# Optimization experiments

Measured on AMD Instinct MI355X. Metric: run time of the kernel, lower is better.

Reference implementation:

```python
import jax, jax.numpy as jnp
import numpy as np

N = 100000   # nodes
E = 1600000  # edges (avg degree 16)
D_IN = 128
H = 256
D_OUT = 128


def setup_inputs() -> dict:
    key = jax.random.key(0)
    ks = jax.random.split(key, 12)

    def lin_w(k, fan_in, fan_out):
        # torch nn.Linear-style uniform init
        bound = 1.0 / np.sqrt(fan_in)
        return jax.random.uniform(k, (fan_in, fan_out), jnp.float32, -bound, bound)

    return {
        "in_feat": jax.random.normal(ks[0], (N, D_IN), jnp.float32),
        "src": jax.random.randint(ks[1], (E,), 0, N, jnp.int32),
        "dst": jax.random.randint(ks[2], (E,), 0, N, jnp.int32),
        "Wc0": lin_w(ks[3], D_IN, H), "bc0": jnp.zeros((H,), jnp.float32),
        "Wc1": lin_w(ks[4], H, H),    "bc1": jnp.zeros((H,), jnp.float32),
        "Wc2": lin_w(ks[5], H, D_OUT),"bc2": jnp.zeros((D_OUT,), jnp.float32),
        "Wr0": lin_w(ks[6], D_OUT, H),"br0": jnp.zeros((H,), jnp.float32),
        "Wr1": lin_w(ks[7], H, H),    "br1": jnp.zeros((H,), jnp.float32),
        "Wr2": lin_w(ks[8], H, D_IN), "br2": jnp.zeros((D_IN,), jnp.float32),
    }


def _graph_conv(h, src, dst, W, b):
    """DGL GraphConv, norm='both': D_out^{-1/2} A D_in^{-1/2} h W + b."""
    ones = jnp.ones(src.shape[0], h.dtype)
    out_deg = jnp.clip(jax.ops.segment_sum(ones, src, num_segments=N), 1.0)
    in_deg = jnp.clip(jax.ops.segment_sum(ones, dst, num_segments=N), 1.0)
    h = h * (out_deg ** -0.5)[:, None]
    h = h @ W                                    # transform before aggregate
    h = jax.ops.segment_sum(h[src], dst, num_segments=N)  # SpMM aggregation
    return h * (in_deg ** -0.5)[:, None] + b


def reference(in_feat, src, dst, Wc0, bc0, Wc1, bc1, Wc2, bc2,
              Wr0, br0, Wr1, br1, Wr2, br2):
    h = jnp.tanh(_graph_conv(in_feat, src, dst, Wc0, bc0))
    h = jnp.tanh(_graph_conv(h, src, dst, Wc1, bc1))
    h = jax.nn.softmax(_graph_conv(h, src, dst, Wc2, bc2), axis=1)
    r = jnp.tanh(h @ Wr0 + br0)
    r = jnp.tanh(r @ Wr1 + br1)
    r = jax.nn.softmax(r @ Wr2 + br2, axis=1)
    return (h, r)
```

## Files before the change

### kernel.cpp

```cpp
#include <hip/hip_runtime.h>

typedef __attribute__((ext_vector_type(8))) short short8;
typedef __attribute__((ext_vector_type(4))) float f32x4;

__device__ __forceinline__ ushort f2bf(float v) {
    unsigned u = __builtin_bit_cast(unsigned, v);
    unsigned r = (u + 0x7FFFu + ((u >> 16) & 1u)) >> 16;
    return (ushort)r;
}
__device__ __forceinline__ float lo16(unsigned p) { return __builtin_bit_cast(float, p << 16); }
__device__ __forceinline__ float hi16(unsigned p) { return __builtin_bit_cast(float, p & 0xFFFF0000u); }

__device__ __forceinline__ float fast_tanh(float x) {
    float cx = fminf(fmaxf(x, -9.f), 9.f);
    float e = __expf(2.f * cx);
    return (e - 1.f) / (e + 1.f);
}

__device__ __forceinline__ void async16(const void* g, void* l) {
    __builtin_amdgcn_global_load_lds(
        (const __attribute__((address_space(1))) unsigned*)g,
        (__attribute__((address_space(3))) unsigned*)l, 16, 0, 0);
}

#define BSHIFT 9
#define CHUNK 4096

__global__ __launch_bounds__(256) void bucket_count(const int* __restrict__ src,
        const int* __restrict__ dst, int* __restrict__ gbc,
        int* __restrict__ outc, int E) {
    __shared__ int cnt[256];
    int t = threadIdx.x;
    cnt[t] = 0;
    __syncthreads();
    int start = blockIdx.x * CHUNK;
    int n = E - start; if (n > CHUNK) n = CHUNK;
#pragma unroll
    for (int k = 0; k < CHUNK / 256; ++k) {
        int i = t + k * 256;
        if (i < n) {
            atomicAdd(&cnt[dst[start + i] >> BSHIFT], 1);
            atomicAdd(&outc[src[start + i]], 1);
        }
    }
    __syncthreads();
    if (cnt[t]) atomicAdd(&gbc[t], cnt[t]);
}

__global__ void scan_buckets(const int* __restrict__ gbc, int* __restrict__ bucketBase,
                             int* __restrict__ pairCursor, int* __restrict__ roff,
                             int N, int E) {
    __shared__ int s[256];
    int t = threadIdx.x;
    int v = gbc[t];
    s[t] = v; __syncthreads();
    for (int o = 1; o < 256; o <<= 1) {
        int y = (t >= o) ? s[t - o] : 0;
        __syncthreads();
        s[t] += y;
        __syncthreads();
    }
    int excl = s[t] - v;
    bucketBase[t] = excl;
    pairCursor[t] = excl;
    if (t == 255) bucketBase[256] = s[255];
    if (t == 0) roff[N] = E;
}

__global__ __launch_bounds__(256) void part_scatter(const int* __restrict__ src,
        const int* __restrict__ dst, int* __restrict__ pairCursor,
        uint2* __restrict__ pairs, int E) {
    __shared__ int cnt[256];
    __shared__ int base[256];
    int t = threadIdx.x;
    cnt[t] = 0;
    __syncthreads();
    int start = blockIdx.x * CHUNK;
    int n = E - start; if (n > CHUNK) n = CHUNK;
    int sv[CHUNK / 256], dv[CHUNK / 256], rk[CHUNK / 256], bk[CHUNK / 256];
#pragma unroll
    for (int k = 0; k < CHUNK / 256; ++k) {
        int i = t + k * 256;
        if (i < n) {
            sv[k] = src[start + i];
            dv[k] = dst[start + i];
            bk[k] = dv[k] >> BSHIFT;
            rk[k] = atomicAdd(&cnt[bk[k]], 1);
        } else bk[k] = -1;
    }
    __syncthreads();
    base[t] = cnt[t] ? atomicAdd(&pairCursor[t], cnt[t]) : 0;
    __syncthreads();
#pragma unroll
    for (int k = 0; k < CHUNK / 256; ++k)
        if (bk[k] >= 0) pairs[base[bk[k]] + rk[k]] = make_uint2((unsigned)sv[k], (unsigned)dv[k]);
}

__global__ __launch_bounds__(256) void build_bucket(const uint2* __restrict__ pairs,
        const int* __restrict__ bucketBase, int* __restrict__ roff,
        float* __restrict__ sIn, int* __restrict__ csr, int N) {
    __shared__ int cnt[512];
    __shared__ int cur[512];
    __shared__ int ss[256];
    int b = blockIdx.x;
    int t = threadIdx.x;
    int lo = b << BSHIFT;
    int s0 = bucketBase[b], s1 = bucketBase[b + 1];
    cnt[t] = 0; cnt[t + 256] = 0;
    __syncthreads();
    for (int j = s0 + t; j < s1; j += 256)
        atomicAdd(&cnt[pairs[j].y - lo], 1);
    __syncthreads();
    int c0 = cnt[2 * t], c1 = cnt[2 * t + 1];
    ss[t] = c0 + c1; __syncthreads();
    for (int o = 1; o < 256; o <<= 1) {
        int y = (t >= o) ? ss[t - o] : 0;
        __syncthreads();
        ss[t] += y;
        __syncthreads();
    }
    int eb = ss[t] - (c0 + c1);
    int p0 = s0 + eb, p1 = s0 + eb + c0;
    cur[2 * t] = p0; cur[2 * t + 1] = p1;
    int n0 = lo + 2 * t, n1 = n0 + 1;
    if (n0 < N) { roff[n0] = p0; sIn[n0] = rsqrtf((float)(c0 > 0 ? c0 : 1)); }
    if (n1 < N) { roff[n1] = p1; sIn[n1] = rsqrtf((float)(c1 > 0 ? c1 : 1)); }
    __syncthreads();
    for (int j = s0 + t; j < s1; j += 256) {
        uint2 p = pairs[j];
        int pos = atomicAdd(&cur[p.y - lo], 1);
        csr[pos] = (int)p.x;
    }
}

__global__ void convw(const float* w0, const float* w1, const float* w2,
                      const float* w3, const float* w4, const float* w5,
                      ushort* __restrict__ Wt) {
    int i = blockIdx.x * 256 + threadIdx.x;
    int base, Km, Nm; const float* W;
    if      (i < 32768)  { base = 0;      Km = 128; Nm = 256; W = w0; }
    else if (i < 98304)  { base = 32768;  Km = 256; Nm = 256; W = w1; }
    else if (i < 131072) { base = 98304;  Km = 256; Nm = 128; W = w2; }
    else if (i < 163840) { base = 131072; Km = 128; Nm = 256; W = w3; }
    else if (i < 229376) { base = 163840; Km = 256; Nm = 256; W = w4; }
    else                 { base = 229376; Km = 256; Nm = 128; W = w5; }
    int l = i - base;
    int k = l / Nm, n = l % Nm;
    Wt[base + n * Km + k] = f2bf(W[l]);
}

__global__ void prescale(const float* __restrict__ x, const int* __restrict__ outc,
                         ushort* __restrict__ o, float* __restrict__ sOut,
                         int total ) {
    int i = blockIdx.x * 256 + threadIdx.x;
    if (i >= total) return;
    int row = i >> 5;
    int oc = outc[row]; if (oc < 1) oc = 1;
    float s = rsqrtf((float)oc);
    if ((i & 31) == 0) sOut[row] = s;
    float4 v = ((const float4*)x)[i];
    ushort4 r;
    r.x = f2bf(v.x * s); r.y = f2bf(v.y * s);
    r.z = f2bf(v.z * s); r.w = f2bf(v.w * s);
    ((ushort4*)o)[i] = r;
}

__global__ __launch_bounds__(256) void agg128(const ushort* __restrict__ F,
        const int* __restrict__ csr, const int* __restrict__ roff,
        const float* __restrict__ sIn, ushort* __restrict__ out, int N) {
    int w = blockIdx.x * 4 + (threadIdx.x >> 6);
    if (w >= N) return;
    int lane = threadIdx.x & 63;
    int b = roff[w], e = roff[w + 1];
    float a0 = 0.f, a1 = 0.f;
    const ushort* base = F + lane * 2;
    int i = b;
    for (; i + 4 <= e; i += 4) {
        int s0 = csr[i], s1 = csr[i + 1], s2 = csr[i + 2], s3 = csr[i + 3];
        unsigned p0 = *(const unsigned*)(base + (size_t)s0 * 128);
        unsigned p1 = *(const unsigned*)(base + (size_t)s1 * 128);
        unsigned p2 = *(const unsigned*)(base + (size_t)s2 * 128);
        unsigned p3 = *(const unsigned*)(base + (size_t)s3 * 128);
        a0 += lo16(p0) + lo16(p1) + lo16(p2) + lo16(p3);
        a1 += hi16(p0) + hi16(p1) + hi16(p2) + hi16(p3);
    }
    for (; i < e; ++i) {
        unsigned p = *(const unsigned*)(base + (size_t)csr[i] * 128);
        a0 += lo16(p); a1 += hi16(p);
    }
    float s = sIn[w];
    ushort2 o2; o2.x = f2bf(a0 * s); o2.y = f2bf(a1 * s);
    *(ushort2*)(out + (size_t)w * 128 + lane * 2) = o2;
}

__global__ __launch_bounds__(256) void agg256(const ushort* __restrict__ F,
        const int* __restrict__ csr, const int* __restrict__ roff,
        const float* __restrict__ sIn, ushort* __restrict__ out, int N) {
    int w = blockIdx.x * 4 + (threadIdx.x >> 6);
    if (w >= N) return;
    int lane = threadIdx.x & 63;
    int b = roff[w], e = roff[w + 1];
    float a0 = 0.f, a1 = 0.f, a2 = 0.f, a3 = 0.f;
    const ushort* base = F + lane * 4;
    int i = b;
    for (; i + 4 <= e; i += 4) {
        int s0 = csr[i], s1 = csr[i + 1], s2 = csr[i + 2], s3 = csr[i + 3];
        uint2 p0 = *(const uint2*)(base + (size_t)s0 * 256);
        uint2 p1 = *(const uint2*)(base + (size_t)s1 * 256);
        uint2 p2 = *(const uint2*)(base + (size_t)s2 * 256);
        uint2 p3 = *(const uint2*)(base + (size_t)s3 * 256);
        a0 += lo16(p0.x) + lo16(p1.x) + lo16(p2.x) + lo16(p3.x);
        a1 += hi16(p0.x) + hi16(p1.x) + hi16(p2.x) + hi16(p3.x);
        a2 += lo16(p0.y) + lo16(p1.y) + lo16(p2.y) + lo16(p3.y);
        a3 += hi16(p0.y) + hi16(p1.y) + hi16(p2.y) + hi16(p3.y);
    }
    for (; i < e; ++i) {
        uint2 p = *(const uint2*)(base + (size_t)csr[i] * 256);
        a0 += lo16(p.x); a1 += hi16(p.x); a2 += lo16(p.y); a3 += hi16(p.y);
    }
    float s = sIn[w];
    ushort4 o4;
    o4.x = f2bf(a0 * s); o4.y = f2bf(a1 * s);
    o4.z = f2bf(a2 * s); o4.w = f2bf(a3 * s);
    *(ushort4*)(out + (size_t)w * 256 + lane * 4) = o4;
}

__global__ __launch_bounds__(256) void agg_softmax(const ushort* __restrict__ F,
        const int* __restrict__ csr, const int* __restrict__ roff,
        const float* __restrict__ sIn, const float* __restrict__ bias,
        float* __restrict__ outh, ushort* __restrict__ outb, int N) {
    int w = blockIdx.x * 4 + (threadIdx.x >> 6);
    if (w >= N) return;
    int lane = threadIdx.x & 63;
    int b = roff[w], e = roff[w + 1];
    float a0 = 0.f, a1 = 0.f;
    const ushort* base = F + lane * 2;
    int i = b;
    for (; i + 4 <= e; i += 4) {
        int s0 = csr[i], s1 = csr[i + 1], s2 = csr[i + 2], s3 = csr[i + 3];
        unsigned p0 = *(const unsigned*)(base + (size_t)s0 * 128);
        unsigned p1 = *(const unsigned*)(base + (size_t)s1 * 128);
        unsigned p2 = *(const unsigned*)(base + (size_t)s2 * 128);
        unsigned p3 = *(const unsigned*)(base + (size_t)s3 * 128);
        a0 += lo16(p0) + lo16(p1) + lo16(p2) + lo16(p3);
        a1 += hi16(p0) + hi16(p1) + hi16(p2) + hi16(p3);
    }
    for (; i < e; ++i) {
        unsigned p = *(const unsigned*)(base + (size_t)csr[i] * 128);
        a0 += lo16(p); a1 += hi16(p);
    }
    float s = sIn[w];
    float2 bb = *(const float2*)(bias + lane * 2);
    float l0 = a0 * s + bb.x, l1 = a1 * s + bb.y;
    float m = fmaxf(l0, l1);
    for (int o = 32; o; o >>= 1) m = fmaxf(m, __shfl_xor(m, o, 64));
    float e0 = __expf(l0 - m), e1 = __expf(l1 - m);
    float sm = e0 + e1;
    for (int o = 32; o; o >>= 1) sm += __shfl_xor(sm, o, 64);
    float inv = 1.f / sm;
    float r0 = e0 * inv, r1 = e1 * inv;
    float2 fo; fo.x = r0; fo.y = r1;
    *(float2*)(outh + (size_t)w * 128 + lane * 2) = fo;
    ushort2 o2; o2.x = f2bf(r0); o2.y = f2bf(r1);
    *(ushort2*)(outb + (size_t)w * 128 + lane * 2) = o2;
}

__global__ __launch_bounds__(256) void softmax_r(const float* __restrict__ L,
                                                 float* __restrict__ out, int N) {
    int w = blockIdx.x * 4 + (threadIdx.x >> 6);
    if (w >= N) return;
    int lane = threadIdx.x & 63;
    const float* row = L + (size_t)w * 128;
    float l0 = row[lane], l1 = row[lane + 64];
    float m = fmaxf(l0, l1);
    for (int o = 32; o; o >>= 1) m = fmaxf(m, __shfl_xor(m, o, 64));
    float e0 = __expf(l0 - m), e1 = __expf(l1 - m);
    float sm = e0 + e1;
    for (int o = 32; o; o >>= 1) sm += __shfl_xor(sm, o, 64);
    float inv = 1.f / sm;
    out[(size_t)w * 128 + lane] = e0 * inv;
    out[(size_t)w * 128 + 64 + lane] = e1 * inv;
}

template <int MODE>
__global__ __launch_bounds__(256) void gemm_kernel(
        const ushort* __restrict__ A, const ushort* __restrict__ Wt,
        const float* __restrict__ bias, const float* __restrict__ rowscale,
        void* __restrict__ out, int M, int K, int Nn) {
    __shared__ ushort ldsA[128 * 64];
    __shared__ ushort ldsB[128 * 64];
    const int tid = threadIdx.x;
    const int lane = tid & 63;
    const int wid = tid >> 6;
    const int rowbase = blockIdx.x * 128;
    const int colbase = blockIdx.y * 128;
    const int wr = (wid >> 1) * 64;
    const int wc = (wid & 1) * 64;

    f32x4 acc[4][4];
#pragma unroll
    for (int i = 0; i < 4; ++i)
#pragma unroll
        for (int j = 0; j < 4; ++j) acc[i][j] = (f32x4){0.f, 0.f, 0.f, 0.f};

    const int sr = lane >> 3;
    const int sp = lane & 7;

    for (int kt = 0; kt < K; kt += 64) {
        __syncthreads();
#pragma unroll
        for (int it = 0; it < 4; ++it) {
            int rl = wid * 32 + it * 8 + sr;
            int grow = rowbase + rl; if (grow > M - 1) grow = M - 1;
            int gca = kt + ((sp ^ (rl & 7)) << 3);
            async16(A + (size_t)grow * K + gca, (char*)ldsA + (wid * 32 + it * 8) * 128);
            int gn = colbase + rl;
            int gcb = kt + ((sp ^ (rl & 7)) << 3);
            async16(Wt + (size_t)gn * K + gcb, (char*)ldsB + (wid * 32 + it * 8) * 128);
        }
        __syncthreads();
        const int l15 = lane & 15, l4 = lane >> 4;
#pragma unroll
        for (int ks = 0; ks < 2; ++ks) {
            short8 af[4], bfr[4];
#pragma unroll
            for (int rt = 0; rt < 4; ++rt) {
                int r = wr + rt * 16 + l15;
                int slot = (ks * 4 + l4) ^ (r & 7);
                af[rt] = *(const short8*)&ldsA[r * 64 + slot * 8];
            }
#pragma unroll
            for (int ct = 0; ct < 4; ++ct) {
                int n = wc + ct * 16 + l15;
                int slot = (ks * 4 + l4) ^ (n & 7);
                bfr[ct] = *(const short8*)&ldsB[n * 64 + slot * 8];
            }
#pragma unroll
            for (int rt = 0; rt < 4; ++rt)
#pragma unroll
                for (int ct = 0; ct < 4; ++ct)
                    acc[rt][ct] = __builtin_amdgcn_mfma_f32_16x16x32_bf16(
                        af[rt], bfr[ct], acc[rt][ct], 0, 0, 0);
        }
    }

    const int l15 = lane & 15, l4 = lane >> 4;
    float bv[4];
#pragma unroll
    for (int ct = 0; ct < 4; ++ct)
        bv[ct] = (MODE != 1 && bias) ? bias[colbase + wc + ct * 16 + l15] : 0.f;
#pragma unroll
    for (int rt = 0; rt < 4; ++rt) {
#pragma unroll
        for (int rg = 0; rg < 4; ++rg) {
            int row = rowbase + wr + rt * 16 + l4 * 4 + rg;
            if (row >= M) continue;
            float sc = 1.f;
            if (MODE == 0 && rowscale) sc = rowscale[row];
#pragma unroll
            for (int ct = 0; ct < 4; ++ct) {
                int col = colbase + wc + ct * 16 + l15;
                float v = acc[rt][ct][rg] + bv[ct];
                if (MODE == 0) v = fast_tanh(v) * sc;
                if (MODE <= 1)
                    ((ushort*)out)[(size_t)row * Nn + col] = f2bf(v);
                else
                    ((float*)out)[(size_t)row * Nn + col] = v;
            }
        }
    }
}

extern "C" void kernel_launch(void* const* d_in, const int* in_sizes, int n_in,
                              void* d_out, int out_size, void* d_ws, size_t ws_size,
                              hipStream_t stream) {
    (void)n_in; (void)out_size; (void)ws_size;
    const float* in_feat = (const float*)d_in[0];
    const int*   src     = (const int*)d_in[1];
    const int*   dstp    = (const int*)d_in[2];
    const float* Wc0 = (const float*)d_in[3];  const float* bc0 = (const float*)d_in[4];
    const float* Wc1 = (const float*)d_in[5];  const float* bc1 = (const float*)d_in[6];
    const float* Wc2 = (const float*)d_in[7];  const float* bc2 = (const float*)d_in[8];
    const float* Wr0 = (const float*)d_in[9];  const float* br0 = (const float*)d_in[10];
    const float* Wr1 = (const float*)d_in[11]; const float* br1 = (const float*)d_in[12];
    const float* Wr2 = (const float*)d_in[13]; const float* br2 = (const float*)d_in[14];

    const int N = in_sizes[0] / 128;
    const int E = in_sizes[1];
    const int numBuckets = (N + ((1 << BSHIFT) - 1)) >> BSHIFT;

    char* ws = (char*)d_ws;
    size_t off = 0;
    auto alloc = [&](size_t bytes) -> char* {
        char* p = ws + off;
        off += (bytes + 255) & ~(size_t)255;
        return p;
    };
    char* S1 = alloc((size_t)N * 256 * 2);
    char* S2 = alloc((size_t)N * 256 * 2);
    int* csr    = (int*)alloc((size_t)E * 4);
    int* roff   = (int*)alloc((size_t)(N + 1) * 4);
    int* outc   = (int*)alloc((size_t)N * 4);
    float* sOut = (float*)alloc((size_t)N * 4);
    float* sIn  = (float*)alloc((size_t)N * 4);
    ushort* Wt  = (ushort*)alloc(262144 * 2);
    int* gbc        = (int*)alloc(256 * 4);
    int* bucketBase = (int*)alloc(257 * 4);
    int* pairCursor = (int*)alloc(256 * 4);
    uint2* pairs = (uint2*)S2;

    hipMemsetAsync(outc, 0, (size_t)N * 4, stream);
    hipMemsetAsync(gbc, 0, 256 * 4, stream);

    int nblk = (E + CHUNK - 1) / CHUNK;
    bucket_count<<<nblk, 256, 0, stream>>>(src, dstp, gbc, outc, E);
    scan_buckets<<<1, 256, 0, stream>>>(gbc, bucketBase, pairCursor, roff, N, E);
    part_scatter<<<nblk, 256, 0, stream>>>(src, dstp, pairCursor, pairs, E);
    build_bucket<<<numBuckets, 256, 0, stream>>>(pairs, bucketBase, roff, sIn, csr, N);

    convw<<<262144 / 256, 256, 0, stream>>>(Wc0, Wc1, Wc2, Wr0, Wr1, Wr2, Wt);

    ushort* Xs = (ushort*)S1;
    prescale<<<(N * 32 + 255) / 256, 256, 0, stream>>>(in_feat, outc, Xs, sOut, N * 32);

    int aggGrid = (N + 3) / 4;
    dim3 g2((N + 127) / 128, 2), g1((N + 127) / 128, 1);

    ushort* A0 = (ushort*)S2;
    agg128<<<aggGrid, 256, 0, stream>>>(Xs, csr, roff, sIn, A0, N);
    ushort* B1 = (ushort*)S1;
    gemm_kernel<0><<<g2, 256, 0, stream>>>(A0, Wt, bc0, sOut, B1, N, 128, 256);
    ushort* A1 = (ushort*)S2;
    agg256<<<aggGrid, 256, 0, stream>>>(B1, csr, roff, sIn, A1, N);
    ushort* B2 = (ushort*)S1;
    gemm_kernel<0><<<g2, 256, 0, stream>>>(A1, Wt + 32768, bc1, sOut, B2, N, 256, 256);
    ushort* T3 = (ushort*)S2;
    gemm_kernel<1><<<g1, 256, 0, stream>>>(B2, Wt + 98304, nullptr, nullptr, T3, N, 256, 128);
    float* outh = (float*)d_out;
    ushort* Hbf = (ushort*)S1;
    agg_softmax<<<aggGrid, 256, 0, stream>>>(T3, csr, roff, sIn, bc2, outh, Hbf, N);
    ushort* R1 = (ushort*)S2;
    gemm_kernel<0><<<g2, 256, 0, stream>>>(Hbf, Wt + 131072, br0, nullptr, R1, N, 128, 256);
    ushort* R2 = (ushort*)S1;
    gemm_kernel<0><<<g2, 256, 0, stream>>>(R1, Wt + 163840, br1, nullptr, R2, N, 256, 256);
    float* logits = (float*)S2;
    gemm_kernel<2><<<g1, 256, 0, stream>>>(R2, Wt + 229376, br2, nullptr, logits, N, 256, 128);
    softmax_r<<<aggGrid, 256, 0, stream>>>(logits, outh + (size_t)N * 128, N);
}
```

Measured before the change: 777.1 us.

## Fuse final softmax into GEMM epilogue and prefetch neighbor indices via shuffles

The last GEMM now computes the row softmax in its epilogue. It uses shuffles plus an LDS cross-warp reduction, which removes the fp32 logits round trip and a separate kernel launch. The three aggregation kernels now load up to 64 neighbor indices with one coalesced load per wave. Each index is broadcast with __shfl, and eight gathers are issued at once for more memory-level parallelism. The extra syncthreads in the epilogue and the shuffle overhead add cost in return.

```diff
diff --git a/kernel.cpp b/kernel.cpp
--- a/kernel.cpp
+++ b/kernel.cpp
@@ -165,6 +165,7 @@
     ((ushort4*)o)[i] = r;
 }
 
+
 __global__ __launch_bounds__(256) void agg128(const ushort* __restrict__ F,
         const int* __restrict__ csr, const int* __restrict__ roff,
         const float* __restrict__ sIn, ushort* __restrict__ out, int N) {
@@ -172,20 +173,30 @@
     if (w >= N) return;
     int lane = threadIdx.x & 63;
     int b = roff[w], e = roff[w + 1];
+    int deg = e - b;
+    int n = deg < 64 ? deg : 64;
     float a0 = 0.f, a1 = 0.f;
-    const ushort* base = F + lane * 2;
-    int i = b;
-    for (; i + 4 <= e; i += 4) {
-        int s0 = csr[i], s1 = csr[i + 1], s2 = csr[i + 2], s3 = csr[i + 3];
-        unsigned p0 = *(const unsigned*)(base + (size_t)s0 * 128);
-        unsigned p1 = *(const unsigned*)(base + (size_t)s1 * 128);
-        unsigned p2 = *(const unsigned*)(base + (size_t)s2 * 128);
-        unsigned p3 = *(const unsigned*)(base + (size_t)s3 * 128);
-        a0 += lo16(p0) + lo16(p1) + lo16(p2) + lo16(p3);
-        a1 += hi16(p0) + hi16(p1) + hi16(p2) + hi16(p3);
-    }
-    for (; i < e; ++i) {
-        unsigned p = *(const unsigned*)(base + (size_t)csr[i] * 128);
+    const char* base = (const char*)(F + lane * 2);
+    int voff = 0;
+    if (n > 0) voff = csr[b + (lane < n ? lane : n - 1)] << 8;
+    int j = 0;
+    for (; j + 8 <= n; j += 8) {
+        unsigned p[8];
+#pragma unroll
+        for (int k = 0; k < 8; ++k) {
+            int o = __shfl(voff, j + k, 64);
+            p[k] = *(const unsigned*)(base + (size_t)(unsigned)o);
+        }
+#pragma unroll
+        for (int k = 0; k < 8; ++k) { a0 += lo16(p[k]); a1 += hi16(p[k]); }
+    }
+    for (; j < n; ++j) {
+        int o = __shfl(voff, j, 64);
+        unsigned p = *(const unsigned*)(base + (size_t)(unsigned)o);
+        a0 += lo16(p); a1 += hi16(p);
+    }
+    for (int i = b + 64; i < e; ++i) {
+        unsigned p = *(const unsigned*)(base + ((size_t)csr[i] << 8));
         a0 += lo16(p); a1 += hi16(p);
     }
     float s = sIn[w];
@@ -200,22 +211,33 @@
     if (w >= N) return;
     int lane = threadIdx.x & 63;
     int b = roff[w], e = roff[w + 1];
+    int deg = e - b;
+    int n = deg < 64 ? deg : 64;
     float a0 = 0.f, a1 = 0.f, a2 = 0.f, a3 = 0.f;
-    const ushort* base = F + lane * 4;
-    int i = b;
-    for (; i + 4 <= e; i += 4) {
-        int s0 = csr[i], s1 = csr[i + 1], s2 = csr[i + 2], s3 = csr[i + 3];
-        uint2 p0 = *(const uint2*)(base + (size_t)s0 * 256);
-        uint2 p1 = *(const uint2*)(base + (size_t)s1 * 256);
-        uint2 p2 = *(const uint2*)(base + (size_t)s2 * 256);
-        uint2 p3 = *(const uint2*)(base + (size_t)s3 * 256);
-        a0 += lo16(p0.x) + lo16(p1.x) + lo16(p2.x) + lo16(p3.x);
-        a1 += hi16(p0.x) + hi16(p1.x) + hi16(p2.x) + hi16(p3.x);
-        a2 += lo16(p0.y) + lo16(p1.y) + lo16(p2.y) + lo16(p3.y);
-        a3 += hi16(p0.y) + hi16(p1.y) + hi16(p2.y) + hi16(p3.y);
-    }
-    for (; i < e; ++i) {
-        uint2 p = *(const uint2*)(base + (size_t)csr[i] * 256);
+    const char* base = (const char*)(F + lane * 4);
+    int voff = 0;
+    if (n > 0) voff = csr[b + (lane < n ? lane : n - 1)] << 9;
+    int j = 0;
+    for (; j + 8 <= n; j += 8) {
+        uint2 p[8];
+#pragma unroll
+        for (int k = 0; k < 8; ++k) {
+            int o = __shfl(voff, j + k, 64);
+            p[k] = *(const uint2*)(base + (size_t)(unsigned)o);
+        }
+#pragma unroll
+        for (int k = 0; k < 8; ++k) {
+            a0 += lo16(p[k].x); a1 += hi16(p[k].x);
+            a2 += lo16(p[k].y); a3 += hi16(p[k].y);
+        }
+    }
+    for (; j < n; ++j) {
+        int o = __shfl(voff, j, 64);
+        uint2 p = *(const uint2*)(base + (size_t)(unsigned)o);
+        a0 += lo16(p.x); a1 += hi16(p.x); a2 += lo16(p.y); a3 += hi16(p.y);
+    }
+    for (int i = b + 64; i < e; ++i) {
+        uint2 p = *(const uint2*)(base + ((size_t)csr[i] << 9));
         a0 += lo16(p.x); a1 += hi16(p.x); a2 += lo16(p.y); a3 += hi16(p.y);
     }
     float s = sIn[w];
@@ -233,20 +255,30 @@
     if (w >= N) return;
     int lane = threadIdx.x & 63;
     int b = roff[w], e = roff[w + 1];
+    int deg = e - b;
+    int n = deg < 64 ? deg : 64;
     float a0 = 0.f, a1 = 0.f;
-    const ushort* base = F + lane * 2;
-    int i = b;
-    for (; i + 4 <= e; i += 4) {
-        int s0 = csr[i], s1 = csr[i + 1], s2 = csr[i + 2], s3 = csr[i + 3];
-        unsigned p0 = *(const unsigned*)(base + (size_t)s0 * 128);
-        unsigned p1 = *(const unsigned*)(base + (size_t)s1 * 128);
-        unsigned p2 = *(const unsigned*)(base + (size_t)s2 * 128);
-        unsigned p3 = *(const unsigned*)(base + (size_t)s3 * 128);
-        a0 += lo16(p0) + lo16(p1) + lo16(p2) + lo16(p3);
-        a1 += hi16(p0) + hi16(p1) + hi16(p2) + hi16(p3);
-    }
-    for (; i < e; ++i) {
-        unsigned p = *(const unsigned*)(base + (size_t)csr[i] * 128);
+    const char* base = (const char*)(F + lane * 2);
+    int voff = 0;
+    if (n > 0) voff = csr[b + (lane < n ? lane : n - 1)] << 8;
+    int j = 0;
+    for (; j + 8 <= n; j += 8) {
+        unsigned p[8];
+#pragma unroll
+        for (int k = 0; k < 8; ++k) {
+            int o = __shfl(voff, j + k, 64);
+            p[k] = *(const unsigned*)(base + (size_t)(unsigned)o);
+        }
+#pragma unroll
+        for (int k = 0; k < 8; ++k) { a0 += lo16(p[k]); a1 += hi16(p[k]); }
+    }
+    for (; j < n; ++j) {
+        int o = __shfl(voff, j, 64);
+        unsigned p = *(const unsigned*)(base + (size_t)(unsigned)o);
+        a0 += lo16(p); a1 += hi16(p);
+    }
+    for (int i = b + 64; i < e; ++i) {
+        unsigned p = *(const unsigned*)(base + ((size_t)csr[i] << 8));
         a0 += lo16(p); a1 += hi16(p);
     }
     float s = sIn[w];
@@ -265,23 +297,6 @@
     *(ushort2*)(outb + (size_t)w * 128 + lane * 2) = o2;
 }
 
-__global__ __launch_bounds__(256) void softmax_r(const float* __restrict__ L,
-                                                 float* __restrict__ out, int N) {
-    int w = blockIdx.x * 4 + (threadIdx.x >> 6);
-    if (w >= N) return;
-    int lane = threadIdx.x & 63;
-    const float* row = L + (size_t)w * 128;
-    float l0 = row[lane], l1 = row[lane + 64];
-    float m = fmaxf(l0, l1);
-    for (int o = 32; o; o >>= 1) m = fmaxf(m, __shfl_xor(m, o, 64));
-    float e0 = __expf(l0 - m), e1 = __expf(l1 - m);
-    float sm = e0 + e1;
-    for (int o = 32; o; o >>= 1) sm += __shfl_xor(sm, o, 64);
-    float inv = 1.f / sm;
-    out[(size_t)w * 128 + lane] = e0 * inv;
-    out[(size_t)w * 128 + 64 + lane] = e1 * inv;
-}
-
 template <int MODE>
 __global__ __launch_bounds__(256) void gemm_kernel(
         const ushort* __restrict__ A, const ushort* __restrict__ Wt,
@@ -349,23 +364,81 @@
 #pragma unroll
     for (int ct = 0; ct < 4; ++ct)
         bv[ct] = (MODE != 1 && bias) ? bias[colbase + wc + ct * 16 + l15] : 0.f;
-#pragma unroll
-    for (int rt = 0; rt < 4; ++rt) {
-#pragma unroll
-        for (int rg = 0; rg < 4; ++rg) {
-            int row = rowbase + wr + rt * 16 + l4 * 4 + rg;
-            if (row >= M) continue;
-            float sc = 1.f;
-            if (MODE == 0 && rowscale) sc = rowscale[row];
-#pragma unroll
-            for (int ct = 0; ct < 4; ++ct) {
-                int col = colbase + wc + ct * 16 + l15;
-                float v = acc[rt][ct][rg] + bv[ct];
-                if (MODE == 0) v = fast_tanh(v) * sc;
-                if (MODE <= 1)
-                    ((ushort*)out)[(size_t)row * Nn + col] = f2bf(v);
-                else
-                    ((float*)out)[(size_t)row * Nn + col] = v;
+
+    if (MODE != 3) {
+#pragma unroll
+        for (int rt = 0; rt < 4; ++rt) {
+#pragma unroll
+            for (int rg = 0; rg < 4; ++rg) {
+                int row = rowbase + wr + rt * 16 + l4 * 4 + rg;
+                if (row >= M) continue;
+                float sc = 1.f;
+                if (MODE == 0 && rowscale) sc = rowscale[row];
+#pragma unroll
+                for (int ct = 0; ct < 4; ++ct) {
+                    int col = colbase + wc + ct * 16 + l15;
+                    float v = acc[rt][ct][rg] + bv[ct];
+                    if (MODE == 0) v = fast_tanh(v) * sc;
+                    if (MODE <= 1)
+                        ((ushort*)out)[(size_t)row * Nn + col] = f2bf(v);
+                    else
+                        ((float*)out)[(size_t)row * Nn + col] = v;
+                }
+            }
+        }
+    } else {
+        __syncthreads();
+        float* sred = (float*)ldsA;
+#pragma unroll
+        for (int rt = 0; rt < 4; ++rt) {
+#pragma unroll
+            for (int rg = 0; rg < 4; ++rg) {
+                float m = acc[rt][0][rg] + bv[0];
+#pragma unroll
+                for (int ct = 1; ct < 4; ++ct) m = fmaxf(m, acc[rt][ct][rg] + bv[ct]);
+                m = fmaxf(m, __shfl_xor(m, 1, 64));
+                m = fmaxf(m, __shfl_xor(m, 2, 64));
+                m = fmaxf(m, __shfl_xor(m, 4, 64));
+                m = fmaxf(m, __shfl_xor(m, 8, 64));
+                int row = wr + rt * 16 + l4 * 4 + rg;
+                if (l15 == 0) sred[(wid & 1) * 128 + row] = m;
+            }
+        }
+        __syncthreads();
+#pragma unroll
+        for (int rt = 0; rt < 4; ++rt) {
+#pragma unroll
+            for (int rg = 0; rg < 4; ++rg) {
+                int row = wr + rt * 16 + l4 * 4 + rg;
+                float m = fmaxf(sred[row], sred[128 + row]);
+                float s = 0.f;
+#pragma unroll
+                for (int ct = 0; ct < 4; ++ct) {
+                    float ev = __expf(acc[rt][ct][rg] + bv[ct] - m);
+                    acc[rt][ct][rg] = ev;
+                    s += ev;
+                }
+                s += __shfl_xor(s, 1, 64);
+                s += __shfl_xor(s, 2, 64);
+                s += __shfl_xor(s, 4, 64);
+                s += __shfl_xor(s, 8, 64);
+                if (l15 == 0) sred[256 + (wid & 1) * 128 + row] = s;
+            }
+        }
+        __syncthreads();
+#pragma unroll
+        for (int rt = 0; rt < 4; ++rt) {
+#pragma unroll
+            for (int rg = 0; rg < 4; ++rg) {
+                int row = wr + rt * 16 + l4 * 4 + rg;
+                float inv = 1.f / (sred[256 + row] + sred[256 + 128 + row]);
+                int grow = rowbase + row;
+                if (grow >= M) continue;
+#pragma unroll
+                for (int ct = 0; ct < 4; ++ct) {
+                    int col = colbase + wc + ct * 16 + l15;
+                    ((float*)out)[(size_t)grow * Nn + col] = acc[rt][ct][rg] * inv;
+                }
             }
         }
     }
@@ -443,7 +516,6 @@
     gemm_kernel<0><<<g2, 256, 0, stream>>>(Hbf, Wt + 131072, br0, nullptr, R1, N, 128, 256);
     ushort* R2 = (ushort*)S1;
     gemm_kernel<0><<<g2, 256, 0, stream>>>(R1, Wt + 163840, br1, nullptr, R2, N, 256, 256);
-    float* logits = (float*)S2;
-    gemm_kernel<2><<<g1, 256, 0, stream>>>(R2, Wt + 229376, br2, nullptr, logits, N, 256, 128);
-    softmax_r<<<aggGrid, 256, 0, stream>>>(logits, outh + (size_t)N * 128, N);
-}
+    gemm_kernel<3><<<g1, 256, 0, stream>>>(R2, Wt + 229376, br2, nullptr,
+                                           outh + (size_t)N * 128, N, 256, 128);
+}
```

After: 735.9 us. 5.3% less time.
